# Performance work log

Hardware: AMD Instinct MI355X
Metric: run time of the kernel (lower is better)

The kernel has to match this reference:

```python
import jax, jax.numpy as jnp
import numpy as np

TAU = 0.5  # init tau
EPS = 1e-8  # F.cosine_similarity eps


def setup_inputs() -> dict:
    key = jax.random.key(0)
    k1, k2 = jax.random.split(key)
    N, D, NUM_CLASSES = 4096, 1024, 128
    layer_embeds = jax.random.normal(k1, (N, D), dtype=jnp.float32)
    y_true = jax.random.randint(k2, (N,), 0, NUM_CLASSES, dtype=jnp.int64)
    return {"layer_embeds": layer_embeds, "y_true": y_true}


def reference(layer_embeds, y_true):
    N = layer_embeds.shape[0]
    # batched cosine similarity, scaled like the original: (cos + 1) * 0.5 * tau
    norms = jnp.maximum(jnp.linalg.norm(layer_embeds, axis=1), EPS)  # [N]
    cos = (layer_embeds @ layer_embeds.T) / (norms[:, None] * norms[None, :])  # [N, N]
    S = (cos + 1.0) * 0.5 * TAU

    same = y_true[:, None] == y_true[None, :]  # [N, N]
    eye = jnp.eye(N, dtype=bool)
    pos_mask = same & ~eye            # same-label pairs, j != i
    neg_mask = ~same                  # different-label pairs (diag excluded since same there)

    # column 0: first positive (in j order), else stays 0
    has_pos = pos_mask.any(axis=1)
    first_pos = jnp.argmax(pos_mask, axis=1)
    pos_val = jnp.where(has_pos, S[jnp.arange(N), first_pos], 0.0)  # [N]

    # negatives fill columns 1.. in j order: col = 1 + (#negatives with j' < j)
    negi = neg_mask.astype(jnp.int32)
    col = 1 + jnp.cumsum(negi, axis=1) - negi  # [N, N]
    W = 2 * N  # pad one dummy column for non-negative entries
    cols = jnp.where(neg_mask, col, W - 1)
    rows = jnp.broadcast_to(jnp.arange(N)[:, None], (N, N))
    loss_temp = jnp.zeros((N, W), dtype=jnp.float32)
    loss_temp = loss_temp.at[rows, cols].set(jnp.where(neg_mask, S, 0.0))
    loss_temp = loss_temp.at[:, 0].set(pos_val)
    loss_temp = loss_temp[:, : 2 * N - 1]  # [N, 2N-1], matches torch buffer

    # -log_softmax, take column 0, sum over rows, divide by N
    lse = jax.nn.logsumexp(loss_temp, axis=1)  # [N]
    loss = jnp.sum(lse - loss_temp[:, 0]) / N
    return loss
```

## Files before the change

kernel.cpp:

```cpp
#include <hip/hip_runtime.h>
#include <hip/hip_bf16.h>
#include <math.h>

#define NN 4096
#define DD 1024
#define NCLS 128
#define TAU 0.5f
#define EPSV 1e-8f
#define NB_GEMM 256
#define NKT 16

typedef __bf16 bf16;
typedef __bf16 bf16x8 __attribute__((ext_vector_type(8)));
typedef __bf16 bf16x4 __attribute__((ext_vector_type(4)));
typedef float f32x4 __attribute__((ext_vector_type(4)));

__device__ __forceinline__ void gl2lds16(const void* g, void* l) {
    __builtin_amdgcn_global_load_lds(
        (const __attribute__((address_space(1))) void*)g,
        (__attribute__((address_space(3))) void*)l,
        16, 0, 0);
}

__global__ __launch_bounds__(256) void k_prep(const float* __restrict__ X,
                                              const int* __restrict__ y,
                                              bf16* __restrict__ Xn,
                                              float* __restrict__ rsum,
                                              float* __restrict__ posv,
                                              int* __restrict__ cnt,
                                              int* __restrict__ fpos) {
    const int t = threadIdx.x;
    if (blockIdx.x == 0) {
        __shared__ int sc[NCLS], s1[NCLS], s2[NCLS];
        if (t < NCLS) { sc[t] = 0; s1[t] = 0x7fffffff; s2[t] = 0x7fffffff; }
        __syncthreads();
        int yv[16];
#pragma unroll
        for (int k = 0; k < 16; ++k) {
            int i = t + k * 256;
            yv[k] = y[i];
            atomicAdd(&sc[yv[k]], 1);
            atomicMin(&s1[yv[k]], i);
        }
        __syncthreads();
#pragma unroll
        for (int k = 0; k < 16; ++k) {
            int i = t + k * 256;
            if (s1[yv[k]] != i) atomicMin(&s2[yv[k]], i);
        }
        __syncthreads();
#pragma unroll
        for (int k = 0; k < 16; ++k) {
            int i = t + k * 256;
            int c = yv[k];
            fpos[i] = (sc[c] >= 2) ? (s1[c] == i ? s2[c] : s1[c]) : -1;
        }
        if (t < NCLS) cnt[t] = sc[t];
        return;
    }
    const int w = t >> 6, lane = t & 63;
    const int row = (blockIdx.x - 1) * 4 + w;
    const float* xr = X + (size_t)row * DD;
    float4 v[4];
    float ss = 0.f;
#pragma unroll
    for (int c = 0; c < 4; ++c) {
        v[c] = *(const float4*)(xr + c * 256 + lane * 4);
        ss += v[c].x * v[c].x + v[c].y * v[c].y + v[c].z * v[c].z + v[c].w * v[c].w;
    }
#pragma unroll
    for (int m = 1; m < 64; m <<= 1) ss += __shfl_xor(ss, m, 64);
    float rn = 1.f / fmaxf(sqrtf(ss), EPSV);
    if (lane == 0) { rsum[row] = 0.f; posv[row] = 0.f; }
#pragma unroll
    for (int c = 0; c < 4; ++c) {
        bf16x4 o;
        o.x = (bf16)(v[c].x * rn);
        o.y = (bf16)(v[c].y * rn);
        o.z = (bf16)(v[c].z * rn);
        o.w = (bf16)(v[c].w * rn);
        *(bf16x4*)(Xn + (size_t)row * DD + c * 256 + lane * 4) = o;
    }
}

__global__ __launch_bounds__(512, 2) void k_gemm(const bf16* __restrict__ Xn,
                                                 const int* __restrict__ y,
                                                 const int* __restrict__ fpos,
                                                 float* __restrict__ rowsum,
                                                 float* __restrict__ posv) {
    __shared__ __align__(16) bf16 As[2][16384];
    __shared__ __align__(16) bf16 Bs[2][16384];

    const int id = (blockIdx.x & 7) * 32 + (blockIdx.x >> 3);
    const int rowA0 = (id >> 4) * 256;
    const int rowB0 = (id & 15) * 256;

    const int tid = threadIdx.x;
    const int lane = tid & 63;
    const int w = tid >> 6;
    const int wm = w & 1, wn = w >> 1;
    const int lr = lane >> 4, lc = lane & 15;

    f32x4 acc[8][4];
#pragma unroll
    for (int i = 0; i < 8; ++i)
#pragma unroll
        for (int j = 0; j < 4; ++j) acc[i][j] = (f32x4){0.f, 0.f, 0.f, 0.f};

    const int rowoff = tid >> 3;
    const int kel = ((tid & 7) ^ (rowoff & 7)) * 8;
    const bf16* gA = Xn + (size_t)(rowA0 + rowoff) * DD + kel;
    const bf16* gB = Xn + (size_t)(rowB0 + rowoff) * DD + kel;

    auto stage_tile = [&](int buf, int k0) {
#pragma unroll
        for (int h = 0; h < 2; ++h)
#pragma unroll
            for (int i = 0; i < 2; ++i) {
                const size_t go = (size_t)(h * 128 + i * 64) * DD + k0;
                const int de = h * 8192 + (i * 512 + tid) * 8;
                gl2lds16(gA + go, &As[buf][de]);
                gl2lds16(gB + go, &Bs[buf][de]);
            }
    };

    const int km = (lc & 7) << 4;
    const int koff0 = ((lr * 16) ^ km) >> 1;
    const int koff1 = ((64 + lr * 16) ^ km) >> 1;
    const int rB = (wn & 1) * 64;

    stage_tile(0, 0);

    for (int t = 0; t < NKT; ++t) {
        asm volatile("s_waitcnt vmcnt(0)" ::: "memory");
        __builtin_amdgcn_s_barrier();
        __builtin_amdgcn_sched_barrier(0);
        const int c = t & 1;
        if (t + 1 < NKT) stage_tile(c ^ 1, (t + 1) * 64);

        const bf16* Abase = &As[c][wm * 8192];
        const bf16* Bbase = &Bs[c][(wn >> 1) * 8192];
        bf16x8 bq0[4], bq1[4];
#pragma unroll
        for (int nt = 0; nt < 4; ++nt) {
            bq0[nt] = *(const bf16x8*)(Bbase + (rB + nt * 16 + lc) * 64 + koff0);
            bq1[nt] = *(const bf16x8*)(Bbase + (rB + nt * 16 + lc) * 64 + koff1);
        }
#pragma unroll
        for (int p = 0; p < 4; ++p) {
            bf16x8 a00 = *(const bf16x8*)(Abase + ((2 * p) * 16 + lc) * 64 + koff0);
            bf16x8 a01 = *(const bf16x8*)(Abase + ((2 * p) * 16 + lc) * 64 + koff1);
            bf16x8 a10 = *(const bf16x8*)(Abase + ((2 * p + 1) * 16 + lc) * 64 + koff0);
            bf16x8 a11 = *(const bf16x8*)(Abase + ((2 * p + 1) * 16 + lc) * 64 + koff1);
            __builtin_amdgcn_s_setprio(1);
#pragma unroll
            for (int nt = 0; nt < 4; ++nt) {
                acc[2 * p][nt] = __builtin_amdgcn_mfma_f32_16x16x32_bf16(a00, bq0[nt], acc[2 * p][nt], 0, 0, 0);
                acc[2 * p][nt] = __builtin_amdgcn_mfma_f32_16x16x32_bf16(a01, bq1[nt], acc[2 * p][nt], 0, 0, 0);
                acc[2 * p + 1][nt] = __builtin_amdgcn_mfma_f32_16x16x32_bf16(a10, bq0[nt], acc[2 * p + 1][nt], 0, 0, 0);
                acc[2 * p + 1][nt] = __builtin_amdgcn_mfma_f32_16x16x32_bf16(a11, bq1[nt], acc[2 * p + 1][nt], 0, 0, 0);
            }
            __builtin_amdgcn_s_setprio(0);
        }
    }

    int ycol[4], cloc[4];
#pragma unroll
    for (int nt = 0; nt < 4; ++nt) {
        cloc[nt] = wn * 64 + nt * 16 + lc;
        ycol[nt] = y[rowB0 + cloc[nt]];
    }
#pragma unroll
    for (int mt = 0; mt < 8; ++mt) {
#pragma unroll
        for (int rr = 0; rr < 4; ++rr) {
            int rloc = wm * 128 + mt * 16 + lr * 4 + rr;
            int rglob = rowA0 + rloc;
            int yrow = y[rglob];
            int fprow = fpos[rglob];
            bool prow = ((unsigned)(fprow - rowB0) < 256u);
            float s = 0.f;
#pragma unroll
            for (int nt = 0; nt < 4; ++nt) {
                float Sv = (acc[mt][nt][rr] + 1.f) * (0.5f * TAU);
                if (prow && rowB0 + cloc[nt] == fprow) posv[rglob] = Sv;
                s += (ycol[nt] != yrow) ? __expf(Sv) : 0.f;
            }
            s += __shfl_xor(s, 1, 16);
            s += __shfl_xor(s, 2, 16);
            s += __shfl_xor(s, 4, 16);
            s += __shfl_xor(s, 8, 16);
            if (lc == 0) atomicAdd(&rowsum[rglob], s);
        }
    }
}

__global__ __launch_bounds__(1024) void k_finalize(const float* __restrict__ rowsum,
                                                   const float* __restrict__ posv,
                                                   const int* __restrict__ y,
                                                   const int* __restrict__ cnt,
                                                   float* __restrict__ out) {
    int t = threadIdx.x;
    float acc = 0.f;
#pragma unroll
    for (int k = 0; k < 4; ++k) {
        int i = t + k * 1024;
        float pv = posv[i];
        float tot = rowsum[i] + __expf(pv) + (float)(NN - 2 + cnt[y[i]]);
        acc += logf(tot) - pv;
    }
#pragma unroll
    for (int m = 1; m < 64; m <<= 1) acc += __shfl_xor(acc, m, 64);
    __shared__ float wsum[16];
    int w = t >> 6, lane = t & 63;
    if (lane == 0) wsum[w] = acc;
    __syncthreads();
    if (t == 0) {
        float s = 0.f;
#pragma unroll
        for (int q = 0; q < 16; ++q) s += wsum[q];
        *out = s / (float)NN;
    }
}

extern "C" void kernel_launch(void* const* d_in, const int* in_sizes, int n_in,
                              void* d_out, int out_size, void* d_ws, size_t ws_size,
                              hipStream_t stream) {
    const float* X = (const float*)d_in[0];
    const int* y = (const int*)d_in[1];
    float* out = (float*)d_out;

    char* ws = (char*)d_ws;
    bf16* Xn    = (bf16*)ws;
    float* rsum = (float*)(ws + 8 * 1024 * 1024);
    float* posv = (float*)(ws + 8 * 1024 * 1024 + 16 * 1024);
    int* cnt    = (int*)(ws + 8 * 1024 * 1024 + 32 * 1024);
    int* fpos   = (int*)(ws + 8 * 1024 * 1024 + 36 * 1024);

    k_prep<<<dim3(NN / 4 + 1), 256, 0, stream>>>(X, y, Xn, rsum, posv, cnt, fpos);
    k_gemm<<<dim3(NB_GEMM), 512, 0, stream>>>(Xn, y, fpos, rsum, posv);
    k_finalize<<<dim3(1), 1024, 0, stream>>>(rsum, posv, y, cnt, out);
}
```

Before: 129.4 us.

## Interleave chunked global-to-LDS staging with quartered MFMA phases in GEMM loop

The k-loop is restructured so each k-tile runs as four MFMA quarters, selected by A-half and B-half. The next tile's global-to-LDS copies are split into four chunks issued between those quarters instead of all at once. A waitcnt of vmcnt(2) at the top of each tile replaces the full drain, so the newest chunk can stay in flight, and explicit lgkmcnt waits separate the LDS register loads from the MFMAs. The aim is to spread memory traffic evenly across the compute phases, at the cost of five barriers per k-tile instead of one and more fragile waitcnt bookkeeping.

```diff
diff --git a/kernel.cpp b/kernel.cpp
--- a/kernel.cpp
+++ b/kernel.cpp
@@ -112,16 +112,12 @@
     const bf16* gA = Xn + (size_t)(rowA0 + rowoff) * DD + kel;
     const bf16* gB = Xn + (size_t)(rowB0 + rowoff) * DD + kel;
 
-    auto stage_tile = [&](int buf, int k0) {
-#pragma unroll
-        for (int h = 0; h < 2; ++h)
-#pragma unroll
-            for (int i = 0; i < 2; ++i) {
-                const size_t go = (size_t)(h * 128 + i * 64) * DD + k0;
-                const int de = h * 8192 + (i * 512 + tid) * 8;
-                gl2lds16(gA + go, &As[buf][de]);
-                gl2lds16(gB + go, &Bs[buf][de]);
-            }
+    auto stage_pair = [&](int buf, int p, int k0) {
+        const int h = p >> 1, i = p & 1;
+        const size_t go = (size_t)(h * 128 + i * 64) * DD + k0;
+        const int de = h * 8192 + (i * 512 + tid) * 8;
+        gl2lds16(gA + go, &As[buf][de]);
+        gl2lds16(gB + go, &Bs[buf][de]);
     };
 
     const int km = (lc & 7) << 4;
@@ -129,40 +125,73 @@
     const int koff1 = ((64 + lr * 16) ^ km) >> 1;
     const int rB = (wn & 1) * 64;
 
-    stage_tile(0, 0);
-
-    for (int t = 0; t < NKT; ++t) {
-        asm volatile("s_waitcnt vmcnt(0)" ::: "memory");
-        __builtin_amdgcn_s_barrier();
-        __builtin_amdgcn_sched_barrier(0);
-        const int c = t & 1;
-        if (t + 1 < NKT) stage_tile(c ^ 1, (t + 1) * 64);
-
+    bf16x8 aA[4][2];
+    bf16x8 bq[2][2][2];
+
+    auto loadA = [&](int c, int qm) {
         const bf16* Abase = &As[c][wm * 8192];
+#pragma unroll
+        for (int mt = 0; mt < 4; ++mt) {
+            const bf16* rp = Abase + ((qm * 4 + mt) * 16 + lc) * 64;
+            aA[mt][0] = *(const bf16x8*)(rp + koff0);
+            aA[mt][1] = *(const bf16x8*)(rp + koff1);
+        }
+    };
+    auto loadB = [&](int c, int qn) {
         const bf16* Bbase = &Bs[c][(wn >> 1) * 8192];
-        bf16x8 bq0[4], bq1[4];
-#pragma unroll
-        for (int nt = 0; nt < 4; ++nt) {
-            bq0[nt] = *(const bf16x8*)(Bbase + (rB + nt * 16 + lc) * 64 + koff0);
-            bq1[nt] = *(const bf16x8*)(Bbase + (rB + nt * 16 + lc) * 64 + koff1);
-        }
-#pragma unroll
-        for (int p = 0; p < 4; ++p) {
-            bf16x8 a00 = *(const bf16x8*)(Abase + ((2 * p) * 16 + lc) * 64 + koff0);
-            bf16x8 a01 = *(const bf16x8*)(Abase + ((2 * p) * 16 + lc) * 64 + koff1);
-            bf16x8 a10 = *(const bf16x8*)(Abase + ((2 * p + 1) * 16 + lc) * 64 + koff0);
-            bf16x8 a11 = *(const bf16x8*)(Abase + ((2 * p + 1) * 16 + lc) * 64 + koff1);
-            __builtin_amdgcn_s_setprio(1);
-#pragma unroll
-            for (int nt = 0; nt < 4; ++nt) {
-                acc[2 * p][nt] = __builtin_amdgcn_mfma_f32_16x16x32_bf16(a00, bq0[nt], acc[2 * p][nt], 0, 0, 0);
-                acc[2 * p][nt] = __builtin_amdgcn_mfma_f32_16x16x32_bf16(a01, bq1[nt], acc[2 * p][nt], 0, 0, 0);
-                acc[2 * p + 1][nt] = __builtin_amdgcn_mfma_f32_16x16x32_bf16(a10, bq0[nt], acc[2 * p + 1][nt], 0, 0, 0);
-                acc[2 * p + 1][nt] = __builtin_amdgcn_mfma_f32_16x16x32_bf16(a11, bq1[nt], acc[2 * p + 1][nt], 0, 0, 0);
+#pragma unroll
+        for (int ntl = 0; ntl < 2; ++ntl) {
+            const bf16* rp = Bbase + (rB + (qn * 2 + ntl) * 16 + lc) * 64;
+            bq[qn][ntl][0] = *(const bf16x8*)(rp + koff0);
+            bq[qn][ntl][1] = *(const bf16x8*)(rp + koff1);
+        }
+    };
+    auto mfma16 = [&](int qm, int qn) {
+        __builtin_amdgcn_s_setprio(1);
+#pragma unroll
+        for (int mt = 0; mt < 4; ++mt)
+#pragma unroll
+            for (int ntl = 0; ntl < 2; ++ntl) {
+                acc[qm * 4 + mt][qn * 2 + ntl] = __builtin_amdgcn_mfma_f32_16x16x32_bf16(
+                    aA[mt][0], bq[qn][ntl][0], acc[qm * 4 + mt][qn * 2 + ntl], 0, 0, 0);
+                acc[qm * 4 + mt][qn * 2 + ntl] = __builtin_amdgcn_mfma_f32_16x16x32_bf16(
+                    aA[mt][1], bq[qn][ntl][1], acc[qm * 4 + mt][qn * 2 + ntl], 0, 0, 0);
             }
-            __builtin_amdgcn_s_setprio(0);
-        }
-    }
+        __builtin_amdgcn_s_setprio(0);
+    };
+
+    auto ktile = [&](int c, int knext, bool stage_on, bool lastWait) {
+        if (stage_on) stage_pair(c ^ 1, 0, knext);
+        if (lastWait) asm volatile("s_waitcnt vmcnt(0)" ::: "memory");
+        else          asm volatile("s_waitcnt vmcnt(2)" ::: "memory");
+        __builtin_amdgcn_s_barrier();
+        loadA(c, 0);
+        loadB(c, 0);
+        asm volatile("s_waitcnt lgkmcnt(0)" ::: "memory");
+        mfma16(0, 0);
+        __builtin_amdgcn_s_barrier();
+        loadB(c, 1);
+        if (stage_on) stage_pair(c ^ 1, 1, knext);
+        asm volatile("s_waitcnt lgkmcnt(0)" ::: "memory");
+        mfma16(0, 1);
+        __builtin_amdgcn_s_barrier();
+        loadA(c, 1);
+        if (stage_on) stage_pair(c ^ 1, 2, knext);
+        asm volatile("s_waitcnt lgkmcnt(0)" ::: "memory");
+        mfma16(1, 0);
+        __builtin_amdgcn_s_barrier();
+        if (stage_on) stage_pair(c ^ 1, 3, knext);
+        mfma16(1, 1);
+        __builtin_amdgcn_s_barrier();
+    };
+
+#pragma unroll
+    for (int p = 0; p < 4; ++p) stage_pair(0, p, 0);
+
+#pragma unroll 2
+    for (int t = 0; t < NKT - 1; ++t)
+        ktile(t & 1, (t + 1) * 64, true, false);
+    ktile((NKT - 1) & 1, 0, false, true);
 
     int ycol[4], cloc[4];
 #pragma unroll
```

After: 126.1 us. 2.6% less time.
